# Optimization experiments

Hardware: AMD Instinct MI355X
Metric: run time of the kernel (lower is better)

Reference implementation:

```python
import jax, jax.numpy as jnp
import numpy as np

T, B, I, H = 4096, 64, 128, 128


def setup_inputs() -> dict:
    key = jax.random.key(0)
    k1, k2, k3, k4, k5 = jax.random.split(key, 5)
    s = 1.0 / np.sqrt(H)
    return {
        "x": jax.random.normal(k1, (T, B, I), dtype=jnp.float32),
        "h0": jnp.zeros((B, H), dtype=jnp.float32),
        "W_ih": jax.random.normal(k2, (H, I), dtype=jnp.float32) * s,
        "W_hh": jax.random.normal(k3, (H, H), dtype=jnp.float32) * s,
        "b_ih": jax.random.normal(k4, (H,), dtype=jnp.float32) * s,
        "b_hh": jax.random.normal(k5, (H,), dtype=jnp.float32) * s,
    }


def reference(x, h0, W_ih, W_hh, b_ih, b_hh):
    # Precompute the input projection for all timesteps in one big GEMM
    # (mathematically identical to per-step x_t @ W_ih^T).
    xp = jnp.einsum("tbi,hi->tbh", x, W_ih) + b_ih  # [T, B, H]

    def step(h, xp_t):
        h = jnp.tanh(xp_t + h @ W_hh.T + b_hh)
        return h, h

    h_final, hs = jax.lax.scan(step, h0, xp)  # hs: [T, B, H]
    return hs, h_final[None]
```

## Files before the change

### kernel.cpp

```cpp
#include <hip/hip_runtime.h>

#define T_N 4096
#define B_N 64
#define I_N 128
#define H_N 128
#define BH  (B_N * H_N)

__global__ __launch_bounds__(256) void xproj_kernel(
    const float* __restrict__ x, const float* __restrict__ Wih,
    const float* __restrict__ bih, float* __restrict__ xp)
{
    __shared__ float wt[I_N][H_N];
    const int tid = threadIdx.x;

    {
        const float4* w4 = (const float4*)Wih;
        #pragma unroll
        for (int it = 0; it < 16; ++it) {
            int i = tid * 16 + it;
            float4 v = w4[i];
            int r = i >> 5;
            int k = (i & 31) << 2;
            wt[k + 0][r] = v.x;
            wt[k + 1][r] = v.y;
            wt[k + 2][r] = v.z;
            wt[k + 3][r] = v.w;
        }
    }
    __syncthreads();

    const int  tx   = tid & 15;
    const int  ty   = tid >> 4;
    const long row0 = (long)blockIdx.x * 128;
    const float* xbase = x + (row0 + ty * 8) * I_N;

    float acc[8][8];
    #pragma unroll
    for (int r = 0; r < 8; ++r)
        #pragma unroll
        for (int c = 0; c < 8; ++c) acc[r][c] = 0.0f;

    #pragma unroll 2
    for (int k4 = 0; k4 < I_N / 4; ++k4) {
        float4 xv[8];
        #pragma unroll
        for (int r = 0; r < 8; ++r)
            xv[r] = *(const float4*)(xbase + r * I_N + k4 * 4);

        #pragma unroll
        for (int kk = 0; kk < 4; ++kk) {
            int k = k4 * 4 + kk;
            float4 w0 = *(const float4*)&wt[k][tx * 4];
            float4 w1 = *(const float4*)&wt[k][64 + tx * 4];
            #pragma unroll
            for (int r = 0; r < 8; ++r) {
                float xk = (kk == 0) ? xv[r].x : (kk == 1) ? xv[r].y
                         : (kk == 2) ? xv[r].z : xv[r].w;
                acc[r][0] = fmaf(xk, w0.x, acc[r][0]);
                acc[r][1] = fmaf(xk, w0.y, acc[r][1]);
                acc[r][2] = fmaf(xk, w0.z, acc[r][2]);
                acc[r][3] = fmaf(xk, w0.w, acc[r][3]);
                acc[r][4] = fmaf(xk, w1.x, acc[r][4]);
                acc[r][5] = fmaf(xk, w1.y, acc[r][5]);
                acc[r][6] = fmaf(xk, w1.z, acc[r][6]);
                acc[r][7] = fmaf(xk, w1.w, acc[r][7]);
            }
        }
    }

    float4 b0 = *(const float4*)(bih + tx * 4);
    float4 b1 = *(const float4*)(bih + 64 + tx * 4);
    #pragma unroll
    for (int r = 0; r < 8; ++r) {
        long row = row0 + ty * 8 + r;
        float4 o0, o1;
        o0.x = acc[r][0] + b0.x;  o0.y = acc[r][1] + b0.y;
        o0.z = acc[r][2] + b0.z;  o0.w = acc[r][3] + b0.w;
        o1.x = acc[r][4] + b1.x;  o1.y = acc[r][5] + b1.y;
        o1.z = acc[r][6] + b1.z;  o1.w = acc[r][7] + b1.w;
        *(float4*)(xp + row * H_N + tx * 4)      = o0;
        *(float4*)(xp + row * H_N + 64 + tx * 4) = o1;
    }
}

__device__ __forceinline__ float tanh_pade(float x) {
    float u = x * x;
    float n = fmaf(u, u + 105.0f, 945.0f);
    float d = fmaf(u, fmaf(15.0f, u, 420.0f), 945.0f);
    float t = x * n * __builtin_amdgcn_rcpf(d);
    return fminf(1.0f, fmaxf(-1.0f, t));
}

#define DPP_XOR1 0xB1
#define DPP_XOR2 0x4E

__device__ __forceinline__ float dpp_add(float v, const int ctrl) {
    int s = __float_as_int(v);
    int r;
    switch (ctrl) {
        case DPP_XOR1: r = __builtin_amdgcn_update_dpp(0, s, DPP_XOR1, 0xF, 0xF, true); break;
        default:       r = __builtin_amdgcn_update_dpp(0, s, DPP_XOR2, 0xF, 0xF, true); break;
    }
    return v + __int_as_float(r);
}

#define DOT4(W4, H4)                                                          \
    fmaf((W4).x, (H4).x, fmaf((W4).y, (H4).y,                                 \
    fmaf((W4).z, (H4).z, (W4).w * (H4).w)))

__global__ __launch_bounds__(512, 1) void scan_kernel(
    const float* __restrict__ Whh, const float* __restrict__ bhh,
    const float* __restrict__ h0, float* __restrict__ out)
{
    const int tid  = threadIdx.x;
    const int b    = blockIdx.x;
    const int lane = tid & 63;
    const int wv   = tid >> 6;
    const int p    = lane & 3;
    const int j    = (lane >> 2) + 16 * wv;
    __shared__ float hbuf[2][4][36];

    float4 w[8];
    #pragma unroll
    for (int c = 0; c < 8; ++c)
        w[c] = *(const float4*)(Whh + j * H_N + 32 * p + 4 * c);

    const float bh = bhh[j];

    if (tid < H_N) hbuf[0][tid >> 5][tid & 31] = h0[b * H_N + tid];

    const float* xq = out + b * H_N + j;
    float*       oq = out + b * H_N + j;

    float xv[4];
    #pragma unroll
    for (int d = 0; d < 4; ++d)
        xv[d] = xq[(size_t)d * BH];

    __syncthreads();

#define RNN_STEP(T0, D, CUR) do {                                             \
        const float4* hb = (const float4*)&hbuf[CUR][p][0];                   \
        float4 hv0 = hb[0], hv1 = hb[1], hv2 = hb[2], hv3 = hb[3];            \
        float4 hv4 = hb[4], hv5 = hb[5], hv6 = hb[6], hv7 = hb[7];            \
        float d01 = DOT4(w[0], hv0) + DOT4(w[1], hv1);                        \
        float d23 = DOT4(w[2], hv2) + DOT4(w[3], hv3);                        \
        float d45 = DOT4(w[4], hv4) + DOT4(w[5], hv5);                        \
        float d67 = DOT4(w[6], hv6) + DOT4(w[7], hv7);                        \
        float s = (d01 + d23) + (d45 + d67);                                  \
        s = dpp_add(s, DPP_XOR1);                                             \
        s = dpp_add(s, DPP_XOR2);                                             \
        float hj;                                                             \
        if (p == 0) {                                                         \
            hj = tanh_pade(s + xv[D] + bh);                                   \
            hbuf[(CUR) ^ 1][j >> 5][j & 31] = hj;                             \
        }                                                                     \
        if ((T0) + 4 < T_N)                                                   \
            xv[D] = xq[(size_t)((T0) + 4) * BH];                              \
        asm volatile("s_waitcnt lgkmcnt(0)" ::: "memory");                    \
        __builtin_amdgcn_s_barrier();                                         \
        if (p == 0) {                                                         \
            oq[(size_t)(T0) * BH] = hj;                                       \
            if ((T0) == T_N - 1) oq[(size_t)T_N * BH] = hj;                   \
        }                                                                     \
        asm volatile("" ::: "memory");                                        \
    } while (0)

    for (int t = 0; t < T_N; t += 4) {
        RNN_STEP(t + 0, 0, 0);
        RNN_STEP(t + 1, 1, 1);
        RNN_STEP(t + 2, 2, 0);
        RNN_STEP(t + 3, 3, 1);
    }
#undef RNN_STEP
}

extern "C" void kernel_launch(void* const* d_in, const int* in_sizes, int n_in,
                              void* d_out, int out_size, void* d_ws, size_t ws_size,
                              hipStream_t stream) {
    const float* x   = (const float*)d_in[0];
    const float* h0  = (const float*)d_in[1];
    const float* Wih = (const float*)d_in[2];
    const float* Whh = (const float*)d_in[3];
    const float* bih = (const float*)d_in[4];
    const float* bhh = (const float*)d_in[5];
    float* out = (float*)d_out;

    xproj_kernel<<<dim3((T_N * B_N) / 128), 256, 0, stream>>>(x, Wih, bih, out);
    scan_kernel<<<dim3(B_N), 512, 0, stream>>>(Whh, bhh, h0, out);
}
```

Before: 1.488 ms.

## Split each hidden unit across two lanes and halve scan block size

```diff
diff --git a/kernel.cpp b/kernel.cpp
--- a/kernel.cpp
+++ b/kernel.cpp
@@ -92,15 +92,10 @@
 }
 
 #define DPP_XOR1 0xB1
-#define DPP_XOR2 0x4E
 
-__device__ __forceinline__ float dpp_add(float v, const int ctrl) {
+__device__ __forceinline__ float dpp_add_xor1(float v) {
     int s = __float_as_int(v);
-    int r;
-    switch (ctrl) {
-        case DPP_XOR1: r = __builtin_amdgcn_update_dpp(0, s, DPP_XOR1, 0xF, 0xF, true); break;
-        default:       r = __builtin_amdgcn_update_dpp(0, s, DPP_XOR2, 0xF, 0xF, true); break;
-    }
+    int r = __builtin_amdgcn_update_dpp(0, s, DPP_XOR1, 0xF, 0xF, true);
     return v + __int_as_float(r);
 }
 
@@ -108,7 +103,7 @@
     fmaf((W4).x, (H4).x, fmaf((W4).y, (H4).y,                                 \
     fmaf((W4).z, (H4).z, (W4).w * (H4).w)))
 
-__global__ __launch_bounds__(512, 1) void scan_kernel(
+__global__ __launch_bounds__(256, 1) void scan_kernel(
     const float* __restrict__ Whh, const float* __restrict__ bhh,
     const float* __restrict__ h0, float* __restrict__ out)
 {
@@ -116,18 +111,18 @@
     const int b    = blockIdx.x;
     const int lane = tid & 63;
     const int wv   = tid >> 6;
-    const int p    = lane & 3;
-    const int j    = (lane >> 2) + 16 * wv;
-    __shared__ float hbuf[2][4][36];
+    const int p    = lane & 1;
+    const int j    = (lane >> 1) + 32 * wv;
+    __shared__ float hbuf[2][2][68];
 
-    float4 w[8];
+    float4 w[16];
     #pragma unroll
-    for (int c = 0; c < 8; ++c)
-        w[c] = *(const float4*)(Whh + j * H_N + 32 * p + 4 * c);
+    for (int c = 0; c < 16; ++c)
+        w[c] = *(const float4*)(Whh + j * H_N + 64 * p + 4 * c);
 
     const float bh = bhh[j];
 
-    if (tid < H_N) hbuf[0][tid >> 5][tid & 31] = h0[b * H_N + tid];
+    if (tid < H_N) hbuf[0][tid >> 6][tid & 63] = h0[b * H_N + tid];
 
     const float* xq = out + b * H_N + j;
     float*       oq = out + b * H_N + j;
@@ -141,28 +136,30 @@
 
 #define RNN_STEP(T0, D, CUR) do {                                             \
         const float4* hb = (const float4*)&hbuf[CUR][p][0];                   \
-        float4 hv0 = hb[0], hv1 = hb[1], hv2 = hb[2], hv3 = hb[3];            \
-        float4 hv4 = hb[4], hv5 = hb[5], hv6 = hb[6], hv7 = hb[7];            \
-        float d01 = DOT4(w[0], hv0) + DOT4(w[1], hv1);                        \
-        float d23 = DOT4(w[2], hv2) + DOT4(w[3], hv3);                        \
-        float d45 = DOT4(w[4], hv4) + DOT4(w[5], hv5);                        \
-        float d67 = DOT4(w[6], hv6) + DOT4(w[7], hv7);                        \
-        float s = (d01 + d23) + (d45 + d67);                                  \
-        s = dpp_add(s, DPP_XOR1);                                             \
-        s = dpp_add(s, DPP_XOR2);                                             \
-        float hj;                                                             \
+        float4 hv0 = hb[0],  hv1 = hb[1],  hv2 = hb[2],  hv3 = hb[3];         \
+        float4 hv4 = hb[4],  hv5 = hb[5],  hv6 = hb[6],  hv7 = hb[7];         \
+        float4 hv8 = hb[8],  hv9 = hb[9],  hvA = hb[10], hvB = hb[11];        \
+        float4 hvC = hb[12], hvD = hb[13], hvE = hb[14], hvF = hb[15];        \
+        float d0 = DOT4(w[0],  hv0) + DOT4(w[1],  hv1);                       \
+        float d1 = DOT4(w[2],  hv2) + DOT4(w[3],  hv3);                       \
+        float d2 = DOT4(w[4],  hv4) + DOT4(w[5],  hv5);                       \
+        float d3 = DOT4(w[6],  hv6) + DOT4(w[7],  hv7);                       \
+        float d4 = DOT4(w[8],  hv8) + DOT4(w[9],  hv9);                       \
+        float d5 = DOT4(w[10], hvA) + DOT4(w[11], hvB);                       \
+        float d6 = DOT4(w[12], hvC) + DOT4(w[13], hvD);                       \
+        float d7 = DOT4(w[14], hvE) + DOT4(w[15], hvF);                       \
+        float s = ((d0 + d1) + (d2 + d3)) + ((d4 + d5) + (d6 + d7));          \
+        s = dpp_add_xor1(s);                                                  \
         if (p == 0) {                                                         \
-            hj = tanh_pade(s + xv[D] + bh);                                   \
-            hbuf[(CUR) ^ 1][j >> 5][j & 31] = hj;                             \
+            float hj = tanh_pade(s + xv[D] + bh);                             \
+            hbuf[(CUR) ^ 1][j >> 6][j & 63] = hj;                             \
+            oq[(size_t)(T0) * BH] = hj;                                       \
+            if ((T0) == T_N - 1) oq[(size_t)T_N * BH] = hj;                   \
         }                                                                     \
         if ((T0) + 4 < T_N)                                                   \
             xv[D] = xq[(size_t)((T0) + 4) * BH];                              \
         asm volatile("s_waitcnt lgkmcnt(0)" ::: "memory");                    \
         __builtin_amdgcn_s_barrier();                                         \
-        if (p == 0) {                                                         \
-            oq[(size_t)(T0) * BH] = hj;                                       \
-            if ((T0) == T_N - 1) oq[(size_t)T_N * BH] = hj;                   \
-        }                                                                     \
         asm volatile("" ::: "memory");                                        \
     } while (0)
 
@@ -187,5 +184,5 @@
     float* out = (float*)d_out;
 
     xproj_kernel<<<dim3((T_N * B_N) / 128), 256, 0, stream>>>(x, Wih, bih, out);
-    scan_kernel<<<dim3(B_N), 512, 0, stream>>>(Whh, bhh, h0, out);
+    scan_kernel<<<dim3(B_N), 256, 0, stream>>>(Whh, bhh, h0, out);
 }
```

Measured after the change: 1.689 ms. +13.5%, slower.
